# Kernel tuning notes

Measured on AMD Instinct MI355X. Metric: run time of the kernel, lower is better.

The kernel has to match this reference:

```python
import jax, jax.numpy as jnp
import numpy as np

D_MODEL = 128
NHEAD = 8
GROUPS = {"s16": (12500, 16), "s64": (3125, 64)}
NEG = -1e9  # finite mask fill: exp(NEG - max) == 0 in fp32, identical softmax for valid keys, no NaNs for fully-padded query rows


def _build_group(nw, L, offset):
    """Deterministic ragged windows: window i holds (i % L) + 1 valid tokens."""
    lengths = (np.arange(nw) % L) + 1
    n = int(lengths.sum())
    win = np.repeat(np.arange(nw), lengths)
    slot = np.arange(n) - np.repeat(np.cumsum(lengths) - lengths, lengths)
    flat_pos = (win * L + slot).astype(np.int32)          # position in flattened [nw*L] padded tensor
    voxel_inds = (np.arange(n) + offset).astype(np.int32)  # rows of feat_2d belonging to this group
    mask = np.ones((nw, L), dtype=bool)
    mask[win, slot] = False                                # True = padded (torch key_padding_mask convention)
    return voxel_inds, flat_pos, mask, n


def setup_inputs() -> dict:
    v16, f16, m16, n16 = _build_group(*GROUPS["s16"], offset=0)
    v64, f64, m64, n64 = _build_group(*GROUPS["s64"], offset=n16)
    N = n16 + n64
    key = jax.random.key(0)
    ks = jax.random.split(key, 8)
    s = 0.02
    return {
        "feat_2d": jax.random.normal(ks[0], (N, D_MODEL), jnp.float32),
        "pos_s16": jax.random.normal(ks[1], (GROUPS["s16"][0], GROUPS["s16"][1], D_MODEL), jnp.float32),
        "pos_s64": jax.random.normal(ks[2], (GROUPS["s64"][0], GROUPS["s64"][1], D_MODEL), jnp.float32),
        "W_in": jax.random.normal(ks[3], (3 * D_MODEL, D_MODEL), jnp.float32) * s,
        "b_in": jax.random.normal(ks[4], (3 * D_MODEL,), jnp.float32) * s,
        "W_out": jax.random.normal(ks[5], (D_MODEL, D_MODEL), jnp.float32) * s,
        "b_out": jax.random.normal(ks[6], (D_MODEL,), jnp.float32) * s,
        "voxel_inds_s16": jnp.asarray(v16), "flat_pos_s16": jnp.asarray(f16),
        "voxel_inds_s64": jnp.asarray(v64), "flat_pos_s64": jnp.asarray(f64),
        "key_padding_s16": jnp.asarray(m16), "key_padding_s64": jnp.asarray(m64),
    }


def _group_attn(feat_2d, pos, W_in, b_in, W_out, b_out, voxel_inds, flat_pos, mask, nw, L):
    C = D_MODEL
    d = C // NHEAD
    # flat2window_v2: scatter flat tokens into padded [nw, L, C]
    feat3d = jnp.zeros((nw * L, C), feat_2d.dtype).at[flat_pos].set(feat_2d[voxel_inds]).reshape(nw, L, C)
    qk_in = feat3d + pos                       # q = k = feat + pos; v = feat
    Wq, Wk, Wv = W_in[:C], W_in[C:2 * C], W_in[2 * C:]
    bq, bk, bv = b_in[:C], b_in[C:2 * C], b_in[2 * C:]
    q = (qk_in @ Wq.T + bq).reshape(nw, L, NHEAD, d)
    k = (qk_in @ Wk.T + bk).reshape(nw, L, NHEAD, d)
    v = (feat3d @ Wv.T + bv).reshape(nw, L, NHEAD, d)
    scale = 1.0 / np.sqrt(d)
    scores = jnp.einsum("nqhd,nkhd->nhqk", q, k) * scale
    scores = jnp.where(mask[:, None, None, :], jnp.asarray(NEG, scores.dtype), scores)
    attn = jax.nn.softmax(scores, axis=-1)
    out = jnp.einsum("nhqk,nkhd->nqhd", attn, v).reshape(nw, L, C)
    out = out @ W_out.T + b_out
    # window2flat_v2: gather valid tokens back out of the padded tensor
    return out.reshape(nw * L, C)[flat_pos]


def reference(feat_2d, pos_s16, pos_s64, W_in, b_in, W_out, b_out,
              voxel_inds_s16, flat_pos_s16, voxel_inds_s64, flat_pos_s64,
              key_padding_s16, key_padding_s64):
    results = jnp.zeros_like(feat_2d)
    o16 = _group_attn(feat_2d, pos_s16, W_in, b_in, W_out, b_out,
                      voxel_inds_s16, flat_pos_s16, key_padding_s16, *GROUPS["s16"])
    o64 = _group_attn(feat_2d, pos_s64, W_in, b_in, W_out, b_out,
                      voxel_inds_s64, flat_pos_s64, key_padding_s64, *GROUPS["s64"])
    results = results.at[voxel_inds_s16].set(o16)
    results = results.at[voxel_inds_s64].set(o64)
    return results
```

## Files before the change

### kernel.cpp

```cpp
#include <hip/hip_runtime.h>
#include <hip/hip_fp16.h>

typedef unsigned short u16;
typedef unsigned int   u32;
typedef _Float16 f16;
typedef f16  f16x4 __attribute__((ext_vector_type(4)));
typedef f16  f16x8 __attribute__((ext_vector_type(8)));
typedef float f32x4 __attribute__((ext_vector_type(4)));

#define MFMA16(A,B,C) __builtin_amdgcn_mfma_f32_16x16x16f16(A,B,C,0,0,0)
#define MFMA32(A,B,C) __builtin_amdgcn_mfma_f32_16x16x32_f16(A,B,C,0,0,0)

static __device__ __forceinline__ int sidx(int r, int c) {
    return (r << 7) + (((c >> 3) ^ (r & 15)) << 3) + (c & 7);
}
static __device__ __forceinline__ int vidx(int d, int t) {
    return (d << 6) + (((t >> 3) ^ (d & 7)) << 3) + (t & 7);
}
static __device__ __forceinline__ u16 f2h(float v) {
    f16 h = (f16)v; u16 u; __builtin_memcpy(&u, &h, 2); return u;
}
static __device__ __forceinline__ u32 pk2(float a, float b) {
    return (u32)f2h(a) | ((u32)f2h(b) << 16);
}

__global__ __launch_bounds__(256)
void conv_w(const float* __restrict__ Win, const float* __restrict__ Wout,
            f16* __restrict__ w1, f16* __restrict__ w2)
{
    int i = blockIdx.x * 256 + threadIdx.x;
    float v = (i < 384 * 128) ? Win[i] : Wout[i - 384 * 128];
    f16 a = (f16)v;
    w1[i] = a;
    w2[i] = (f16)((v - (float)a) * 2048.0f);
}

static __device__ __forceinline__
void proj128(const u16* src, u16* dst,
             const f16* __restrict__ w1, const f16* __restrict__ w2,
             const float* __restrict__ bias, int lo, int g, int wv)
{
    const int col = wv * 16 + lo;
    f16x8 B1[4], B2[4];
    #pragma unroll
    for (int ks = 0; ks < 4; ++ks) {
        B1[ks] = *(const f16x8*)(w1 + col * 128 + ks * 32 + g * 8);
        B2[ks] = *(const f16x8*)(w2 + col * 128 + ks * 32 + g * 8);
    }
    const float bv = bias[col];
    f32x4 a1[4], a2[4];
    #pragma unroll
    for (int m = 0; m < 4; ++m) {
        a1[m] = (f32x4){bv, bv, bv, bv};
        a2[m] = (f32x4){0.f, 0.f, 0.f, 0.f};
    }
    #pragma unroll
    for (int ks = 0; ks < 4; ++ks) {
        #pragma unroll
        for (int m = 0; m < 4; ++m) {
            f16x8 A = *(const f16x8*)&src[sidx(m * 16 + lo, ks * 32 + g * 8)];
            a1[m] = MFMA32(A, B1[ks], a1[m]);
            a2[m] = MFMA32(A, B2[ks], a2[m]);
        }
    }
    #pragma unroll
    for (int m = 0; m < 4; ++m)
        #pragma unroll
        for (int r = 0; r < 4; ++r)
            dst[sidx(m * 16 + 4 * g + r, col)] =
                f2h(a1[m][r] + a2[m][r] * (1.0f / 2048.0f));
}

static __device__ __forceinline__
void vt_gemm(const u16* src, u16* dst,
             const f16* __restrict__ w1, const f16* __restrict__ w2,
             const float* __restrict__ bias, int lo, int g, int wv)
{
    const int d0 = wv * 16;
    f16x8 A1[4], A2[4];
    #pragma unroll
    for (int ks = 0; ks < 4; ++ks) {
        A1[ks] = *(const f16x8*)(w1 + (d0 + lo) * 128 + ks * 32 + g * 8);
        A2[ks] = *(const f16x8*)(w2 + (d0 + lo) * 128 + ks * 32 + g * 8);
    }
    f32x4 bv;
    #pragma unroll
    for (int r = 0; r < 4; ++r) bv[r] = bias[d0 + 4 * g + r];
    f32x4 a1[4], a2[4];
    #pragma unroll
    for (int nt = 0; nt < 4; ++nt) {
        a1[nt] = bv;
        a2[nt] = (f32x4){0.f, 0.f, 0.f, 0.f};
    }
    #pragma unroll
    for (int ks = 0; ks < 4; ++ks) {
        #pragma unroll
        for (int nt = 0; nt < 4; ++nt) {
            f16x8 B = *(const f16x8*)&src[sidx(nt * 16 + lo, ks * 32 + g * 8)];
            a1[nt] = MFMA32(A1[ks], B, a1[nt]);
            a2[nt] = MFMA32(A2[ks], B, a2[nt]);
        }
    }
    #pragma unroll
    for (int nt = 0; nt < 4; ++nt)
        #pragma unroll
        for (int r = 0; r < 4; ++r)
            dst[vidx(d0 + 4 * g + r, nt * 16 + lo)] =
                f2h(a1[nt][r] + a2[nt][r] * (1.0f / 2048.0f));
}

template<int L>
static __device__ __forceinline__
void out_proj(const u16* src,
              const f16* __restrict__ w1, const f16* __restrict__ w2,
              const float* __restrict__ bias, float* __restrict__ out,
              long tok0, int rr0, int lo, int g, int wv)
{
    const int col = wv * 16 + lo;
    f16x8 B1[4], B2[4];
    #pragma unroll
    for (int ks = 0; ks < 4; ++ks) {
        B1[ks] = *(const f16x8*)(w1 + col * 128 + ks * 32 + g * 8);
        B2[ks] = *(const f16x8*)(w2 + col * 128 + ks * 32 + g * 8);
    }
    const float bv = bias[col];
    f32x4 a1[4], a2[4];
    #pragma unroll
    for (int m = 0; m < 4; ++m) {
        a1[m] = (f32x4){bv, bv, bv, bv};
        a2[m] = (f32x4){0.f, 0.f, 0.f, 0.f};
    }
    #pragma unroll
    for (int ks = 0; ks < 4; ++ks) {
        #pragma unroll
        for (int m = 0; m < 4; ++m) {
            f16x8 A = *(const f16x8*)&src[sidx(m * 16 + lo, ks * 32 + g * 8)];
            a1[m] = MFMA32(A, B1[ks], a1[m]);
            a2[m] = MFMA32(A, B2[ks], a2[m]);
        }
    }
    #pragma unroll
    for (int m = 0; m < 4; ++m) {
        const int j    = (L == 16) ? m : 0;
        const int lenj = rr0 + j + 1;
        const long base = tok0 + ((L == 16)
                          ? (long)(j * (rr0 + 1) + ((j * (j - 1)) >> 1)) : 0L);
        #pragma unroll
        for (int r = 0; r < 4; ++r) {
            const int row  = m * 16 + 4 * g + r;
            const int slot = row & (L - 1);
            if (slot < lenj)
                out[(base + slot) * 128 + col] =
                    a1[m][r] + a2[m][r] * (1.0f / 2048.0f);
        }
    }
}

template<int L>
static __device__ __forceinline__
void body(const float* __restrict__ feat,
          const float* __restrict__ pos,
          const f16*  __restrict__ w1,
          const f16*  __restrict__ w2,
          const float* __restrict__ bin,
          const float* __restrict__ bout,
          float* __restrict__ out,
          int goff, int w0, int nw, u16* lds)
{
    constexpr int LSH = (L == 16) ? 4 : 6;
    u16* bufA = lds;
    u16* bufB = lds + 8192;
    u16* bufC = lds + 16384;
    u16* bufD = lds + 24576;

    const int tid  = threadIdx.x;
    const int wv   = tid >> 6;
    const int lane = tid & 63;
    const int lo   = lane & 15;
    const int g    = lane >> 4;

    if (w0 >= nw) return;
    const int rr0 = w0 & (L - 1);
    const long start = (long)w0 + (long)(w0 >> LSH) * (L * (L - 1) / 2)
                     + (long)((rr0 * (rr0 - 1)) >> 1);
    const long tok0 = (long)goff + start;

    #pragma unroll
    for (int it = 0; it < 2; ++it) {
        const int ch  = tid + it * 512;
        const int row = ch >> 4, c8 = (ch & 15) << 3;
        const int j    = (L == 16) ? (row >> 4) : 0;
        const int slot = row & (L - 1);
        float4 fa = make_float4(0.f, 0.f, 0.f, 0.f), fb = fa;
        if (slot < rr0 + j + 1) {
            const int cumj = j * (rr0 + 1) + ((j * (j - 1)) >> 1);
            const float* s = feat + (tok0 + cumj + slot) * 128 + c8;
            fa = *(const float4*)s;
            fb = *(const float4*)(s + 4);
        }
        const float* pp = pos + ((long)w0 * L + row) * 128 + c8;
        float4 pa = *(const float4*)pp;
        float4 pb = *(const float4*)(pp + 4);
        uint4 xf, xq;
        xf.x = pk2(fa.x, fa.y);           xf.y = pk2(fa.z, fa.w);
        xf.z = pk2(fb.x, fb.y);           xf.w = pk2(fb.z, fb.w);
        xq.x = pk2(fa.x + pa.x, fa.y + pa.y);
        xq.y = pk2(fa.z + pa.z, fa.w + pa.w);
        xq.z = pk2(fb.x + pb.x, fb.y + pb.y);
        xq.w = pk2(fb.z + pb.z, fb.w + pb.w);
        *(uint4*)&bufA[sidx(row, c8)] = xf;
        *(uint4*)&bufB[sidx(row, c8)] = xq;
    }
    __syncthreads();

    vt_gemm(bufA, bufC, w1 + 256 * 128, w2 + 256 * 128, bin + 256, lo, g, wv);
    proj128(bufB, bufD, w1, w2, bin, lo, g, wv);
    __syncthreads();

    proj128(bufB, bufA, w1 + 128 * 128, w2 + 128 * 128, bin + 128, lo, g, wv);
    __syncthreads();

    const f32x4 zf = {0.f, 0.f, 0.f, 0.f};
    if constexpr (L == 16) {
        const int j  = wv >> 1;
        const int lj = rr0 + j + 1;
        const int h0 = (wv & 1) * 4;
        #pragma unroll
        for (int hh = 0; hh < 4; ++hh) {
            const int h = h0 + hh;
            f16x4 Kf = *(const f16x4*)&bufA[sidx(j * 16 + lo, h * 16 + g * 4)];
            f16x4 Qf = *(const f16x4*)&bufD[sidx(j * 16 + lo, h * 16 + g * 4)];
            f32x4 S = MFMA16(Kf, Qf, zf);
            float p[4]; float mx = -3.0e38f;
            #pragma unroll
            for (int r = 0; r < 4; ++r) {
                const int key = 4 * g + r;
                p[r] = (key < lj) ? S[r] * 0.25f : -1.0e9f;
                mx = fmaxf(mx, p[r]);
            }
            mx = fmaxf(mx, __shfl_xor(mx, 16, 64));
            mx = fmaxf(mx, __shfl_xor(mx, 32, 64));
            float sum = 0.f;
            #pragma unroll
            for (int r = 0; r < 4; ++r) { p[r] = __expf(p[r] - mx); sum += p[r]; }
            sum += __shfl_xor(sum, 16, 64);
            sum += __shfl_xor(sum, 32, 64);
            const float inv = 1.0f / sum;
            f16x4 Pf = { (f16)(p[0]*inv), (f16)(p[1]*inv),
                         (f16)(p[2]*inv), (f16)(p[3]*inv) };
            f16x4 Vf = *(const f16x4*)&bufC[vidx(h * 16 + lo, j * 16 + g * 4)];
            f32x4 O = MFMA16(Pf, Vf, zf);
            #pragma unroll
            for (int r = 0; r < 4; ++r)
                bufB[sidx(j * 16 + 4 * g + r, h * 16 + lo)] = f2h(O[r]);
        }
    } else {
        const int lj = rr0 + 1;
        const int h  = wv;
        f16x4 Kf[4], Vf[4];
        #pragma unroll
        for (int kt = 0; kt < 4; ++kt)
            Kf[kt] = *(const f16x4*)&bufA[sidx(kt * 16 + lo, h * 16 + g * 4)];
        #pragma unroll
        for (int kt = 0; kt < 4; ++kt)
            Vf[kt] = *(const f16x4*)&bufC[vidx(h * 16 + lo, kt * 16 + g * 4)];
        #pragma unroll
        for (int qt = 0; qt < 4; ++qt) {
            f16x4 Qf = *(const f16x4*)&bufD[sidx(qt * 16 + lo, h * 16 + g * 4)];
            f32x4 S[4];
            #pragma unroll
            for (int kt = 0; kt < 4; ++kt) S[kt] = MFMA16(Kf[kt], Qf, zf);
            float p[16]; float mx = -3.0e38f;
            #pragma unroll
            for (int kt = 0; kt < 4; ++kt)
                #pragma unroll
                for (int r = 0; r < 4; ++r) {
                    const int key = kt * 16 + 4 * g + r;
                    float v = (key < lj) ? S[kt][r] * 0.25f : -1.0e9f;
                    p[kt * 4 + r] = v; mx = fmaxf(mx, v);
                }
            mx = fmaxf(mx, __shfl_xor(mx, 16, 64));
            mx = fmaxf(mx, __shfl_xor(mx, 32, 64));
            float sum = 0.f;
            #pragma unroll
            for (int i = 0; i < 16; ++i) { p[i] = __expf(p[i] - mx); sum += p[i]; }
            sum += __shfl_xor(sum, 16, 64);
            sum += __shfl_xor(sum, 32, 64);
            const float inv = 1.0f / sum;
            f32x4 acc = zf;
            #pragma unroll
            for (int kt = 0; kt < 4; ++kt) {
                f16x4 Pf = { (f16)(p[kt*4+0]*inv), (f16)(p[kt*4+1]*inv),
                             (f16)(p[kt*4+2]*inv), (f16)(p[kt*4+3]*inv) };
                acc = MFMA16(Pf, Vf[kt], acc);
            }
            #pragma unroll
            for (int r = 0; r < 4; ++r)
                bufB[sidx(qt * 16 + 4 * g + r, h * 16 + lo)] = f2h(acc[r]);
        }
    }
    __syncthreads();

    out_proj<L>(bufB, w1 + 384 * 128, w2 + 384 * 128, bout, out,
                tok0, rr0, lo, g, wv);
}

__global__ __launch_bounds__(512, 4)
void win_attn_all(const float* __restrict__ feat,
                  const float* __restrict__ pos16,
                  const float* __restrict__ pos64,
                  const f16*  __restrict__ w1,
                  const f16*  __restrict__ w2,
                  const float* __restrict__ bin,
                  const float* __restrict__ bout,
                  float* __restrict__ out,
                  int nb16, int nw16, int nw64, int n16)
{
    __shared__ __align__(16) u16 lds[32768];
    const int bid = (int)blockIdx.x;
    if (bid < nb16)
        body<16>(feat, pos16, w1, w2, bin, bout, out, 0,   bid * 4,     nw16, lds);
    else
        body<64>(feat, pos64, w1, w2, bin, bout, out, n16, bid - nb16,  nw64, lds);
}

extern "C" void kernel_launch(void* const* d_in, const int* in_sizes, int n_in,
                              void* d_out, int out_size, void* d_ws, size_t ws_size,
                              hipStream_t stream)
{
    (void)n_in; (void)out_size; (void)ws_size;
    const float* feat  = (const float*)d_in[0];
    const float* pos16 = (const float*)d_in[1];
    const float* pos64 = (const float*)d_in[2];
    const float* Win   = (const float*)d_in[3];
    const float* bin   = (const float*)d_in[4];
    const float* Wout  = (const float*)d_in[5];
    const float* bout  = (const float*)d_in[6];
    float* out = (float*)d_out;
    const int n16  = in_sizes[7];
    const int nw16 = in_sizes[1] / (16 * 128);
    const int nw64 = in_sizes[2] / (64 * 128);
    const int nb16 = (nw16 + 3) / 4;

    f16* w1 = (f16*)d_ws;
    f16* w2 = w1 + 512 * 128;

    hipLaunchKernelGGL(conv_w, dim3(256), dim3(256), 0, stream, Win, Wout, w1, w2);
    hipLaunchKernelGGL(win_attn_all, dim3(nb16 + nw64), dim3(512), 0, stream,
                       feat, pos16, pos64, w1, w2, bin, bout, out,
                       nb16, nw16, nw64, n16);
}
```

Measured before the change: 503.3 us.

## Keep Q and K projections in registers, shrink LDS, raise occupancy

Q and K projections are now computed in transposed form, so each wave holds its own head's Q and K fragments directly in registers. This removes the LDS round-trip and one barrier between projections. The LDS footprint drops from four buffers to three, and the launch bounds ask for 6 blocks per SIMD group instead of 4, aiming at more resident blocks. The risk is higher register pressure from holding the qf/kf/vf fragments, and the nw bounds check was removed, which assumes nw16 is a multiple of 4.

```diff
diff --git a/kernel.cpp b/kernel.cpp
--- a/kernel.cpp
+++ b/kernel.cpp
@@ -20,6 +20,9 @@
 static __device__ __forceinline__ u16 f2h(float v) {
     f16 h = (f16)v; u16 u; __builtin_memcpy(&u, &h, 2); return u;
 }
+static __device__ __forceinline__ u16 h2u(f16 h) {
+    u16 u; __builtin_memcpy(&u, &h, 2); return u;
+}
 static __device__ __forceinline__ u32 pk2(float a, float b) {
     return (u32)f2h(a) | ((u32)f2h(b) << 16);
 }
@@ -36,45 +39,10 @@
 }
 
 static __device__ __forceinline__
-void proj128(const u16* src, u16* dst,
-             const f16* __restrict__ w1, const f16* __restrict__ w2,
-             const float* __restrict__ bias, int lo, int g, int wv)
-{
-    const int col = wv * 16 + lo;
-    f16x8 B1[4], B2[4];
-    #pragma unroll
-    for (int ks = 0; ks < 4; ++ks) {
-        B1[ks] = *(const f16x8*)(w1 + col * 128 + ks * 32 + g * 8);
-        B2[ks] = *(const f16x8*)(w2 + col * 128 + ks * 32 + g * 8);
-    }
-    const float bv = bias[col];
-    f32x4 a1[4], a2[4];
-    #pragma unroll
-    for (int m = 0; m < 4; ++m) {
-        a1[m] = (f32x4){bv, bv, bv, bv};
-        a2[m] = (f32x4){0.f, 0.f, 0.f, 0.f};
-    }
-    #pragma unroll
-    for (int ks = 0; ks < 4; ++ks) {
-        #pragma unroll
-        for (int m = 0; m < 4; ++m) {
-            f16x8 A = *(const f16x8*)&src[sidx(m * 16 + lo, ks * 32 + g * 8)];
-            a1[m] = MFMA32(A, B1[ks], a1[m]);
-            a2[m] = MFMA32(A, B2[ks], a2[m]);
-        }
-    }
-    #pragma unroll
-    for (int m = 0; m < 4; ++m)
-        #pragma unroll
-        for (int r = 0; r < 4; ++r)
-            dst[sidx(m * 16 + 4 * g + r, col)] =
-                f2h(a1[m][r] + a2[m][r] * (1.0f / 2048.0f));
-}
-
-static __device__ __forceinline__
-void vt_gemm(const u16* src, u16* dst,
-             const f16* __restrict__ w1, const f16* __restrict__ w2,
-             const float* __restrict__ bias, int lo, int g, int wv)
+void gemmT_regs(const u16* src,
+                const f16* __restrict__ w1, const f16* __restrict__ w2,
+                const float* __restrict__ bias,
+                int lo, int g, int wv, f16x4* of)
 {
     const int d0 = wv * 16;
     f16x8 A1[4], A2[4];
@@ -102,11 +70,13 @@
         }
     }
     #pragma unroll
-    for (int nt = 0; nt < 4; ++nt)
+    for (int nt = 0; nt < 4; ++nt) {
+        f16x4 o;
         #pragma unroll
         for (int r = 0; r < 4; ++r)
-            dst[vidx(d0 + 4 * g + r, nt * 16 + lo)] =
-                f2h(a1[nt][r] + a2[nt][r] * (1.0f / 2048.0f));
+            o[r] = (f16)(a1[nt][r] + a2[nt][r] * (1.0f / 2048.0f));
+        of[nt] = o;
+    }
 }
 
 template<int L>
@@ -165,13 +135,12 @@
           const float* __restrict__ bin,
           const float* __restrict__ bout,
           float* __restrict__ out,
-          int goff, int w0, int nw, u16* lds)
+          int goff, int w0, u16* lds)
 {
     constexpr int LSH = (L == 16) ? 4 : 6;
-    u16* bufA = lds;
-    u16* bufB = lds + 8192;
+    u16* bufF = lds;
+    u16* bufX = lds + 8192;
     u16* bufC = lds + 16384;
-    u16* bufD = lds + 24576;
 
     const int tid  = threadIdx.x;
     const int wv   = tid >> 6;
@@ -179,7 +148,6 @@
     const int lo   = lane & 15;
     const int g    = lane >> 4;
 
-    if (w0 >= nw) return;
     const int rr0 = w0 & (L - 1);
     const long start = (long)w0 + (long)(w0 >> LSH) * (L * (L - 1) / 2)
                      + (long)((rr0 * (rr0 - 1)) >> 1);
@@ -208,29 +176,28 @@
         xq.y = pk2(fa.z + pa.z, fa.w + pa.w);
         xq.z = pk2(fb.x + pb.x, fb.y + pb.y);
         xq.w = pk2(fb.z + pb.z, fb.w + pb.w);
-        *(uint4*)&bufA[sidx(row, c8)] = xf;
-        *(uint4*)&bufB[sidx(row, c8)] = xq;
+        *(uint4*)&bufF[sidx(row, c8)] = xf;
+        *(uint4*)&bufX[sidx(row, c8)] = xq;
     }
     __syncthreads();
 
-    vt_gemm(bufA, bufC, w1 + 256 * 128, w2 + 256 * 128, bin + 256, lo, g, wv);
-    proj128(bufB, bufD, w1, w2, bin, lo, g, wv);
-    __syncthreads();
-
-    proj128(bufB, bufA, w1 + 128 * 128, w2 + 128 * 128, bin + 128, lo, g, wv);
+    f16x4 vf[4], qf[4], kf[4];
+    gemmT_regs(bufF, w1 + 256 * 128, w2 + 256 * 128, bin + 256, lo, g, wv, vf);
+    #pragma unroll
+    for (int nt = 0; nt < 4; ++nt)
+        #pragma unroll
+        for (int r = 0; r < 4; ++r)
+            bufC[vidx(wv * 16 + 4 * g + r, nt * 16 + lo)] = h2u(vf[nt][r]);
+    gemmT_regs(bufX, w1,             w2,             bin,       lo, g, wv, qf);
+    gemmT_regs(bufX, w1 + 128 * 128, w2 + 128 * 128, bin + 128, lo, g, wv, kf);
     __syncthreads();
 
     const f32x4 zf = {0.f, 0.f, 0.f, 0.f};
     if constexpr (L == 16) {
-        const int j  = wv >> 1;
-        const int lj = rr0 + j + 1;
-        const int h0 = (wv & 1) * 4;
-        #pragma unroll
-        for (int hh = 0; hh < 4; ++hh) {
-            const int h = h0 + hh;
-            f16x4 Kf = *(const f16x4*)&bufA[sidx(j * 16 + lo, h * 16 + g * 4)];
-            f16x4 Qf = *(const f16x4*)&bufD[sidx(j * 16 + lo, h * 16 + g * 4)];
-            f32x4 S = MFMA16(Kf, Qf, zf);
+        #pragma unroll
+        for (int j = 0; j < 4; ++j) {
+            const int lj = rr0 + j + 1;
+            f32x4 S = MFMA16(kf[j], qf[j], zf);
             float p[4]; float mx = -3.0e38f;
             #pragma unroll
             for (int r = 0; r < 4; ++r) {
@@ -248,28 +215,23 @@
             const float inv = 1.0f / sum;
             f16x4 Pf = { (f16)(p[0]*inv), (f16)(p[1]*inv),
                          (f16)(p[2]*inv), (f16)(p[3]*inv) };
-            f16x4 Vf = *(const f16x4*)&bufC[vidx(h * 16 + lo, j * 16 + g * 4)];
+            f16x4 Vf = *(const f16x4*)&bufC[vidx(wv * 16 + lo, j * 16 + g * 4)];
             f32x4 O = MFMA16(Pf, Vf, zf);
             #pragma unroll
             for (int r = 0; r < 4; ++r)
-                bufB[sidx(j * 16 + 4 * g + r, h * 16 + lo)] = f2h(O[r]);
+                bufX[sidx(j * 16 + 4 * g + r, wv * 16 + lo)] = f2h(O[r]);
         }
     } else {
         const int lj = rr0 + 1;
-        const int h  = wv;
-        f16x4 Kf[4], Vf[4];
+        f16x4 Vf[4];
         #pragma unroll
         for (int kt = 0; kt < 4; ++kt)
-            Kf[kt] = *(const f16x4*)&bufA[sidx(kt * 16 + lo, h * 16 + g * 4)];
-        #pragma unroll
-        for (int kt = 0; kt < 4; ++kt)
-            Vf[kt] = *(const f16x4*)&bufC[vidx(h * 16 + lo, kt * 16 + g * 4)];
+            Vf[kt] = *(const f16x4*)&bufC[vidx(wv * 16 + lo, kt * 16 + g * 4)];
         #pragma unroll
         for (int qt = 0; qt < 4; ++qt) {
-            f16x4 Qf = *(const f16x4*)&bufD[sidx(qt * 16 + lo, h * 16 + g * 4)];
             f32x4 S[4];
             #pragma unroll
-            for (int kt = 0; kt < 4; ++kt) S[kt] = MFMA16(Kf[kt], Qf, zf);
+            for (int kt = 0; kt < 4; ++kt) S[kt] = MFMA16(kf[kt], qf[qt], zf);
             float p[16]; float mx = -3.0e38f;
             #pragma unroll
             for (int kt = 0; kt < 4; ++kt)
@@ -296,16 +258,16 @@
             }
             #pragma unroll
             for (int r = 0; r < 4; ++r)
-                bufB[sidx(qt * 16 + 4 * g + r, h * 16 + lo)] = f2h(acc[r]);
+                bufX[sidx(qt * 16 + 4 * g + r, wv * 16 + lo)] = f2h(acc[r]);
         }
     }
     __syncthreads();
 
-    out_proj<L>(bufB, w1 + 384 * 128, w2 + 384 * 128, bout, out,
+    out_proj<L>(bufX, w1 + 384 * 128, w2 + 384 * 128, bout, out,
                 tok0, rr0, lo, g, wv);
 }
 
-__global__ __launch_bounds__(512, 4)
+__global__ __launch_bounds__(512, 6)
 void win_attn_all(const float* __restrict__ feat,
                   const float* __restrict__ pos16,
                   const float* __restrict__ pos64,
@@ -314,14 +276,14 @@
                   const float* __restrict__ bin,
                   const float* __restrict__ bout,
                   float* __restrict__ out,
-                  int nb16, int nw16, int nw64, int n16)
-{
-    __shared__ __align__(16) u16 lds[32768];
+                  int nb16, int n16)
+{
+    __shared__ __align__(16) u16 lds[24576];
     const int bid = (int)blockIdx.x;
     if (bid < nb16)
-        body<16>(feat, pos16, w1, w2, bin, bout, out, 0,   bid * 4,     nw16, lds);
+        body<16>(feat, pos16, w1, w2, bin, bout, out, 0,   bid * 4,    lds);
     else
-        body<64>(feat, pos64, w1, w2, bin, bout, out, n16, bid - nb16,  nw64, lds);
+        body<64>(feat, pos64, w1, w2, bin, bout, out, n16, bid - nb16, lds);
 }
 
 extern "C" void kernel_launch(void* const* d_in, const int* in_sizes, int n_in,
@@ -348,5 +310,5 @@
     hipLaunchKernelGGL(conv_w, dim3(256), dim3(256), 0, stream, Win, Wout, w1, w2);
     hipLaunchKernelGGL(win_attn_all, dim3(nb16 + nw64), dim3(512), 0, stream,
                        feat, pos16, pos64, w1, w2, bin, bout, out,
-                       nb16, nw16, nw64, n16);
-}
+                       nb16, n16);
+}
```

New measurement: 807.3 us. 60.4% more time.
